# Performance work log

Hardware: AMD Instinct MI355X
Metric: run time of the kernel (lower is better)

Reference implementation:

```python
import jax, jax.numpy as jnp
import numpy as np

L = 8          # context_length
P = 196        # patches_per_frame
PT = 16        # patches_per_tactile_frame
N_EMBD = 768
N_HEAD = 12
BATCH = 4
T = (L + 1) + L * PT + L * P  # 1705


def build_mask(L, P, Pt):
    # image-query block rows (L*P rows)
    mi = np.zeros((L * P, L * P))
    a1 = np.zeros((L * P, L + 1))
    t1 = np.zeros((L * P, L * Pt))
    for i in range(L):
        mi[i * P:(i + 1) * P, :(i + 1) * P] = 1
        a1[i * P:(i + 2) * P, :i + 2] = 1
        t1[i * P:(i + 1) * P, :(i + 1) * Pt] = 1
    m1 = np.concatenate([a1, t1, mi], axis=1)
    # tactile-query block rows (L*Pt rows)
    a2 = np.zeros((L * Pt, L + 1))
    t2 = np.zeros((L * Pt, L * Pt))
    i2 = np.zeros((L * Pt, L * P))
    for i in range(L):
        a2[i * Pt:(i + 2) * Pt, :i + 2] = 1
        t2[i * Pt:(i + 1) * Pt, :(i + 1) * Pt] = 1
        i2[i * Pt:(i + 1) * Pt, :(i + 1) * P] = 1
    m2 = np.concatenate([a2, t2, i2], axis=1)
    # action-query rows (L+1 rows)
    a3 = np.zeros((L + 1, L + 1))
    t3 = np.zeros((L + 1, L * Pt))
    i3 = np.zeros((L + 1, L * P))
    for i in range(L + 1):
        a3[i:i + 2, :i + 2] = 1
        t3[i:i + 1, :(i + 1) * Pt] = 1
        i3[i:i + 1, :(i + 1) * P] = 1
    m3 = np.concatenate([a3, t3, i3], axis=1)
    return np.concatenate([m3, m2, m1], axis=0).astype(bool)


def setup_inputs() -> dict:
    key = jax.random.key(0)
    k1, k2, k3 = jax.random.split(key, 3)
    x = jax.random.normal(k1, (BATCH, T, N_EMBD), dtype=jnp.float32)
    W_attn = jax.random.normal(k2, (N_EMBD, 3 * N_EMBD), dtype=jnp.float32) * 0.02
    W_proj = jax.random.normal(k3, (N_EMBD, N_EMBD), dtype=jnp.float32) * 0.02
    mask = jnp.asarray(build_mask(L, P, PT))
    return {"x": x, "W_attn": W_attn, "W_proj": W_proj, "mask": mask, "n_head": N_HEAD}


def reference(x, W_attn, W_proj, mask, n_head):
    B, Tq, C = x.shape
    hd = C // n_head
    qkv = x @ W_attn                      # [B, T, 3C]
    q, k, v = jnp.split(qkv, 3, axis=-1)
    # [B, H, T, hd]
    q = q.reshape(B, Tq, n_head, hd).transpose(0, 2, 1, 3)
    k = k.reshape(B, Tq, n_head, hd).transpose(0, 2, 1, 3)
    v = v.reshape(B, Tq, n_head, hd).transpose(0, 2, 1, 3)
    scores = jnp.einsum("bhqd,bhkd->bhqk", q, k) / jnp.sqrt(jnp.float32(hd))
    scores = jnp.where(mask[None, None, :, :], scores, jnp.float32(-1e9))
    probs = jax.nn.softmax(scores, axis=-1)
    y = jnp.einsum("bhqk,bhkd->bhqd", probs, v)
    y = y.transpose(0, 2, 1, 3).reshape(B, Tq, C)
    return y @ W_proj
```

## Files before the change

### kernel.cpp

```cpp
#include <hip/hip_runtime.h>
#include <hip/hip_bf16.h>

typedef __attribute__((ext_vector_type(8))) short short8;
typedef __attribute__((ext_vector_type(4))) float f32x4;

#define MFMA16(a,b,c) __builtin_amdgcn_mfma_f32_16x16x32_bf16((a),(b),(c),0,0,0)

#define WAITVM(N) asm volatile("s_waitcnt vmcnt(" #N ")" ::: "memory")
#define BAR()     asm volatile("s_barrier" ::: "memory")

constexpr int Tt = 1705;
constexpr int Tp = 1792;
constexpr int NKT_ALL = 28;
constexpr int NH = 12, HD = 64, Bb = 4, C_ = 768;
constexpr int M_  = Bb * Tt;
constexpr int Mp  = 6912;
constexpr int NQT = 14;
constexpr int NCH = 4;
constexpr float QSCALE = 0.18033688011116016f;

static_assert(Mp % 256 == 0 && (3 * C_) % 256 == 0, "256-tile grid");

__device__ __forceinline__ void gl16(const void* g, void* l) {
  __builtin_amdgcn_global_load_lds((const __attribute__((address_space(1))) void*)g,
                                   (__attribute__((address_space(3))) void*)l, 16, 0, 0);
}

__device__ __forceinline__ float ex2(float x) {
  float r; asm("v_exp_f32 %0, %1" : "=v"(r) : "v"(x)); return r;
}

__device__ __forceinline__ int frame_of(int t) {
  return t < 9 ? t : (t < 137 ? ((t - 9) >> 4) : ((t - 137) / 196));
}

__device__ __forceinline__ int lim16(int a) {
  if (a >= Tt) return 0;
  int bnd = min(a + 15, Tt - 1);
  int fmax = (a == 0) ? 8 : frame_of(min(bnd, a < 137 ? 136 : bnd));
  return (fmax >= 8) ? Tt : 137 + (fmax + 1) * 196;
}

constexpr int PREP_CONV = Mp * C_ / 4 / 256;
constexpr int PREP_TA   = (C_ / 32) * (3 * C_ / 32);
constexpr int PREP_TB   = (C_ / 32) * (C_ / 32);

__global__ __launch_bounds__(256) void k_prep(const float* __restrict__ x,
                                              __hip_bfloat16* __restrict__ xb,
                                              const float* __restrict__ Wa,
                                              __hip_bfloat16* __restrict__ wat,
                                              const float* __restrict__ Wp,
                                              __hip_bfloat16* __restrict__ wpt) {
  __shared__ float tile[32][33];
  const int bid = blockIdx.x, tid = threadIdx.x;
  if (bid < PREP_CONV) {
    int i = bid * 256 + tid;
    float4 v = make_float4(0.f, 0.f, 0.f, 0.f);
    if (i * 4 < M_ * C_) v = ((const float4*)x)[i];
    __hip_bfloat16 o0 = __float2bfloat16(v.x), o1 = __float2bfloat16(v.y),
                   o2 = __float2bfloat16(v.z), o3 = __float2bfloat16(v.w);
    ushort4 u = make_ushort4(*(unsigned short*)&o0, *(unsigned short*)&o1,
                             *(unsigned short*)&o2, *(unsigned short*)&o3);
    ((ushort4*)xb)[i] = u;
    return;
  }
  const float* src; __hip_bfloat16* dst; int N, bid2;
  if (bid < PREP_CONV + PREP_TA) { bid2 = bid - PREP_CONV; src = Wa; dst = wat; N = 3 * C_; }
  else                           { bid2 = bid - PREP_CONV - PREP_TA; src = Wp; dst = wpt; N = C_; }
  const int K = C_;
  int kb = (bid2 % (C_ / 32)) * 32, nb = (bid2 / (C_ / 32)) * 32;
  int tx = tid & 31, ty = tid >> 5;
  for (int i = 0; i < 4; i++)
    tile[ty + i * 8][tx] = src[(size_t)(kb + ty + i * 8) * N + nb + tx];
  __syncthreads();
  for (int i = 0; i < 4; i++)
    dst[(size_t)(nb + ty + i * 8) * K + kb + tx] = __float2bfloat16(tile[tx][ty + i * 8]);
}

__global__ __launch_bounds__(512) void k_gemm_qkv(const __hip_bfloat16* __restrict__ xb,
                                                  const __hip_bfloat16* __restrict__ wat,
                                                  __hip_bfloat16* __restrict__ q,
                                                  __hip_bfloat16* __restrict__ kpk,
                                                  __hip_bfloat16* __restrict__ vpk) {
  __shared__ __hip_bfloat16 smem[65536];
  const int tid = threadIdx.x;
  const int lane = tid & 63, w = tid >> 6;
  const int wr = w >> 2, wc = w & 3;
  const int l16 = lane & 15, grp = lane >> 4;
  const int m0 = blockIdx.x * 256, n0 = blockIdx.y * 256;
  constexpr int NT = C_ / 32;
  constexpr int ES = 132;

  auto stage = [&](int t, int bb) {
    int k0 = t * 32;
    __hip_bfloat16* As = smem + bb * 8192;
    __hip_bfloat16* Bs = smem + 32768 + bb * 8192;
    for (int p = 0; p < 2; p++) {
      int idx = p * 512 + tid;
      int row = idx >> 2;
      int c8 = (idx & 3) ^ ((row >> 1) & 3);
      gl16(xb  + (size_t)(m0 + row) * C_ + k0 + c8 * 8, As + idx * 8);
      gl16(wat + (size_t)(n0 + row) * C_ + k0 + c8 * 8, Bs + idx * 8);
    }
  };

  f32x4 acc[8][4];
  for (int i = 0; i < 8; i++)
    for (int j = 0; j < 4; j++) { f32x4 z = {0.f,0.f,0.f,0.f}; acc[i][j] = z; }

  stage(0, 0); stage(1, 1); stage(2, 2);

  for (int t = 0; t < NT; t++) {
    if (t + 3 < NT) stage(t + 3, (t + 3) & 3);
    int rem = NT - 1 - t;
    if (rem >= 3)      WAITVM(12);
    else if (rem == 2) WAITVM(8);
    else if (rem == 1) WAITVM(4);
    else               WAITVM(0);
    BAR();
    const __hip_bfloat16* Ac = smem + (t & 3) * 8192;
    const __hip_bfloat16* Bc = smem + 32768 + (t & 3) * 8192;
    short8 bfr[4], afr[4];
    for (int nj = 0; nj < 4; nj++) {
      int row = wc * 64 + nj * 16 + l16;
      bfr[nj] = *(const short8*)(Bc + row * 32 + ((grp ^ ((row >> 1) & 3)) * 8));
    }
    for (int mi = 0; mi < 4; mi++) {
      int row = wr * 128 + mi * 16 + l16;
      afr[mi] = *(const short8*)(Ac + row * 32 + ((grp ^ ((row >> 1) & 3)) * 8));
    }
    __builtin_amdgcn_s_setprio(1);
    for (int mi = 0; mi < 4; mi++)
      for (int nj = 0; nj < 4; nj++)
        acc[mi][nj] = MFMA16(afr[mi], bfr[nj], acc[mi][nj]);
    __builtin_amdgcn_s_setprio(0);
    for (int mi = 0; mi < 4; mi++) {
      int row = wr * 128 + 64 + mi * 16 + l16;
      afr[mi] = *(const short8*)(Ac + row * 32 + ((grp ^ ((row >> 1) & 3)) * 8));
    }
    __builtin_amdgcn_s_setprio(1);
    for (int mi = 0; mi < 4; mi++)
      for (int nj = 0; nj < 4; nj++)
        acc[4 + mi][nj] = MFMA16(afr[mi], bfr[nj], acc[4 + mi][nj]);
    __builtin_amdgcn_s_setprio(0);
    BAR();
  }

  const int which = n0 / C_;
  const int cbase = n0 - which * C_;
  const int h0 = cbase >> 6;
  const float scale = (which == 0) ? QSCALE : 1.0f;
  const int b0 = m0 / Tt;
  const int b1 = min((m0 + 255) / Tt, Bb - 1);
  __hip_bfloat16* epi = smem;

  const int mmD = tid & 15, ggD = (tid >> 4) & 3;
  const int loD = (tid >> 6) & 1, hiD = tid >> 7;
  const int tinK = hiD * 16 + mmD, dK = loD * 32 + ggD * 8;
  const int dV = hiD * 16 + mmD;

  for (int pc = 0; pc < 2; pc++) {
    if ((wc >> 1) == pc) {
      int colw = (wc & 1) * 64;
      for (int mi = 0; mi < 8; mi++)
        for (int nj = 0; nj < 4; nj++) {
          int row = wr * 128 + mi * 16 + grp * 4;
          int col = colw + nj * 16 + l16;
          #pragma unroll
          for (int r = 0; r < 4; r++)
            epi[(row + r) * ES + col] = __float2bfloat16(acc[mi][nj][r] * scale);
        }
    }
    __syncthreads();
    for (int b = b0; b <= b1; b++) {
      int ts = max(0, m0 - b * Tt), te = min(Tt, m0 + 256 - b * Tt);
      if (ts >= te) continue;
      const int rb = b * Tt - m0;
      if (which == 0) {
        for (int hh = 0; hh < 2; hh++) {
          int bh = b * NH + h0 + pc * 2 + hh;
          __hip_bfloat16* qd = q + (size_t)bh * Tp * HD;
          for (int tc = ts & ~63; tc < te; tc += 64) {
            int t = tc + (tid >> 3);
            int d0 = (tid & 7) * 8;
            if (t >= ts && t < te) {
              int ad = (rb + t) * ES + hh * 64 + d0;
              union { short8 v; ushort4 h[2]; } u;
              u.h[0] = *(const ushort4*)(epi + ad);
              u.h[1] = *(const ushort4*)(epi + ad + 4);
              *(short8*)(qd + (size_t)t * HD + d0) = u.v;
            }
          }
        }
      } else if (which == 1) {
        for (int kt = ts >> 6; kt <= (te - 1) >> 6; kt++)
          for (int hh = 0; hh < 2; hh++) {
            int bh = b * NH + h0 + pc * 2 + hh;
            int t = kt * 64 + tinK;
            if (t >= ts && t < te) {
              int ad = (rb + t) * ES + hh * 64 + dK;
              union { short8 v; ushort4 h[2]; } u;
              u.h[0] = *(const ushort4*)(epi + ad);
              u.h[1] = *(const ushort4*)(epi + ad + 4);
              ((short8*)(kpk + ((size_t)bh * NKT_ALL + kt) * 4096))[tid] = u.v;
            }
          }
      } else {
        for (int kt = ts >> 6; kt <= (te - 1) >> 6; kt++)
          for (int hh = 0; hh < 2; hh++) {
            int bh = b * NH + h0 + pc * 2 + hh;
            __hip_bfloat16* vd = vpk + ((size_t)bh * NKT_ALL + kt) * 4096;
            bool full = (kt * 64 >= ts) && (kt * 64 + 64 <= te);
            if (full) {
              short8 v;
              #pragma unroll
              for (int s = 0; s < 8; s++) {
                int tin = loD * 32 + ggD * 4 + (s & 3) + ((s >> 2) << 4);
                v[s] = *(const short*)(epi + (rb + kt * 64 + tin) * ES + hh * 64 + dV);
              }
              ((short8*)vd)[tid] = v;
            } else {
              #pragma unroll
              for (int s = 0; s < 8; s++) {
                int tin = loD * 32 + ggD * 4 + (s & 3) + ((s >> 2) << 4);
                int t = kt * 64 + tin;
                if (t >= ts && t < te)
                  vd[tid * 8 + s] = epi[(rb + t) * ES + hh * 64 + dV];
              }
            }
          }
      }
    }
    __syncthreads();
  }
}

__global__ __launch_bounds__(256) void k_gemm_proj128(const __hip_bfloat16* __restrict__ A,
                                                      const __hip_bfloat16* __restrict__ Bt,
                                                      float* __restrict__ out) {
  __shared__ __hip_bfloat16 As[4][128 * 32], Bs[4][128 * 32];
  const int tid = threadIdx.x;
  const int lane = tid & 63, w = tid >> 6;
  const int wr = w >> 1, wc = w & 1;
  const int l16 = lane & 15, grp = lane >> 4;
  const int m0 = blockIdx.x * 128, n0 = blockIdx.y * 128;
  constexpr int NT = C_ / 32;

  auto stage = [&](int t, int bb) {
    int k0 = t * 32;
    for (int p = 0; p < 2; p++) {
      int idx = p * 256 + tid;
      int row = idx >> 2;
      int c8 = (idx & 3) ^ ((row >> 1) & 3);
      gl16(A  + (size_t)(m0 + row) * C_ + k0 + c8 * 8, &As[bb][idx * 8]);
      gl16(Bt + (size_t)(n0 + row) * C_ + k0 + c8 * 8, &Bs[bb][idx * 8]);
    }
  };

  f32x4 acc[4][4];
  for (int i = 0; i < 4; i++)
    for (int j = 0; j < 4; j++) { f32x4 z = {0.f,0.f,0.f,0.f}; acc[i][j] = z; }

  stage(0, 0); stage(1, 1); stage(2, 2);

  for (int t = 0; t < NT; t++) {
    if (t + 3 < NT) stage(t + 3, (t + 3) & 3);
    int rem = NT - 1 - t;
    if (rem >= 3)      WAITVM(12);
    else if (rem == 2) WAITVM(8);
    else if (rem == 1) WAITVM(4);
    else               WAITVM(0);
    BAR();
    const __hip_bfloat16* Ac = As[t & 3];
    const __hip_bfloat16* Bc = Bs[t & 3];
    short8 afr[4], bfr[4];
    for (int nj = 0; nj < 4; nj++) {
      int row = wc * 64 + nj * 16 + l16;
      bfr[nj] = *(const short8*)(Bc + row * 32 + ((grp ^ ((row >> 1) & 3)) * 8));
    }
    for (int mi = 0; mi < 4; mi++) {
      int row = wr * 64 + mi * 16 + l16;
      afr[mi] = *(const short8*)(Ac + row * 32 + ((grp ^ ((row >> 1) & 3)) * 8));
    }
    __builtin_amdgcn_s_setprio(1);
    for (int mi = 0; mi < 4; mi++)
      for (int nj = 0; nj < 4; nj++)
        acc[mi][nj] = MFMA16(afr[mi], bfr[nj], acc[mi][nj]);
    __builtin_amdgcn_s_setprio(0);
    BAR();
  }

  for (int mi = 0; mi < 4; mi++)
    for (int r = 0; r < 4; r++) {
      int m = m0 + wr * 64 + mi * 16 + grp * 4 + r;
      if (m >= M_) continue;
      for (int nj = 0; nj < 4; nj++)
        out[(size_t)m * C_ + n0 + wc * 64 + nj * 16 + l16] = acc[mi][nj][r];
    }
}

union S8u { short8 v; struct { unsigned long long lo, hi; } q; unsigned u[4]; };

__device__ __forceinline__ unsigned pack2bf(float a, float b) {
  union { __hip_bfloat162 h; unsigned u; } cv;
  cv.h = __float22bfloat162_rn(make_float2(a, b));
  return cv.u;
}

__constant__ int QLUT[NQT] = {0, 1, 11, 12, 13, 10, 8, 9, 7, 5, 6, 4, 2, 3};

__global__ __launch_bounds__(256, 2) void k_attn(const __hip_bfloat16* __restrict__ q,
                                                 const __hip_bfloat16* __restrict__ kpk,
                                                 const __hip_bfloat16* __restrict__ vpk,
                                                 __hip_bfloat16* __restrict__ Opart,
                                                 float* __restrict__ lpart) {
  const int tid = threadIdx.x, lane = tid & 63, w = tid >> 6;
  const int l16 = lane & 15, grp = lane >> 4;
  const int id = blockIdx.x;
  const int xslot = id & 7, rr_ = id >> 3;
  const int bh = xslot + 8 * (rr_ / 56);
  const int cqs = rr_ % 56;
  const int qt = QLUT[cqs >> 2], ch = cqs & (NCH - 1);
  const int cq = qt * NCH + ch;
  const int t0q = qt * 128;
  const __hip_bfloat16* qb = q + (size_t)bh * Tp * HD;

  int lim[2], Cmn[2], Ath[2], Bth[2], Cth[2];
  for (int g = 0; g < 2; g++) {
    int a = t0q + w * 32 + g * 16;
    lim[g] = lim16(a);
    int fqmn, fql;
    if (a >= Tt) { fqmn = 8; fql = 8; }
    else {
      int bnd = min(a + 15, Tt - 1);
      fqmn = min(frame_of(a), frame_of(bnd));
      int t = a + l16;
      fql = (t >= Tt) ? 8 : frame_of(t);
    }
    Cmn[g] = min(137 + 196 * (fqmn + 1), Tt);
    Ath[g] = fql + 2;
    Bth[g] = 9 + 16 * (fql + 1);
    Cth[g] = min(137 + 196 * (fql + 1), Tt);
  }
  int limw = max(lim[0], lim[1]);
  int nktw = (limw + 63) >> 6;
  int k0t = (ch * nktw) >> 2;
  int k1t = ((ch + 1) * nktw) >> 2;

  short8 qa[2][2];
  for (int g = 0; g < 2; g++) {
    const __hip_bfloat16* qr = qb + (size_t)(t0q + w * 32 + g * 16 + l16) * HD + grp * 8;
    qa[g][0] = *(const short8*)(qr);
    qa[g][1] = *(const short8*)(qr + 32);
  }
  f32x4 o[2][4];
  for (int g = 0; g < 2; g++)
    for (int jt = 0; jt < 4; jt++) { f32x4 z = {0.f,0.f,0.f,0.f}; o[g][jt] = z; }
  f32x4 ps[2];
  { f32x4 z = {0.f,0.f,0.f,0.f}; ps[0] = z; ps[1] = z; }

  const short8* kbase = (const short8*)(kpk + (size_t)bh * NKT_ALL * 4096);
  const short8* vbase = (const short8*)(vpk + (size_t)bh * NKT_ALL * 4096);

  for (int kt = k0t; kt < k1t; kt++) {
    const int t0k = kt * 64;
    const short8* kp = kbase + (size_t)kt * 512;
    const short8* vp = vbase + (size_t)kt * 512;
    short8 kf[4][2], vf[4][2];
    for (int j = 0; j < 4; j++)
      for (int hh = 0; hh < 2; hh++) kf[j][hh] = kp[(j * 2 + hh) * 64 + lane];
    for (int jt = 0; jt < 4; jt++)
      for (int kb2 = 0; kb2 < 2; kb2++) vf[jt][kb2] = vp[(jt * 2 + kb2) * 64 + lane];

    f32x4 s[2][4];
    for (int j = 0; j < 4; j++) {
      f32x4 z = {0.f,0.f,0.f,0.f};
      s[0][j] = MFMA16(kf[j][0], qa[0][0], z);
      s[0][j] = MFMA16(kf[j][1], qa[0][1], s[0][j]);
      s[1][j] = MFMA16(kf[j][0], qa[1][0], z);
      s[1][j] = MFMA16(kf[j][1], qa[1][1], s[1][j]);
    }

    bool act0 = t0k < lim[0], act1 = t0k < lim[1];
    bool fullk = (t0k + 64 <= Tt);
    S8u pf[2][2];
    for (int g = 0; g < 2; g++) {
      bool act = g == 0 ? act0 : act1;
      if (!act) continue;
      bool needm = !(fullk && (t0k >= 192 ? (t0k + 64) <= Cmn[g] : Cmn[g] >= Tt));
      if (needm) {
        for (int j = 0; j < 4; j++)
          for (int r = 0; r < 4; r++) {
            int key = t0k + j * 16 + grp * 4 + r;
            int thr = key < 9 ? Ath[g] : (key < 137 ? Bth[g] : Cth[g]);
            if (key >= thr) s[g][j][r] = -1e30f;
          }
      }
      f32x4 p[4];
      for (int j = 0; j < 4; j++)
        for (int r = 0; r < 4; r++) p[j][r] = ex2(s[g][j][r]);
      ps[g] += (p[0] + p[1]) + (p[2] + p[3]);
      pf[g][0].u[0] = pack2bf(p[0][0], p[0][1]);
      pf[g][0].u[1] = pack2bf(p[0][2], p[0][3]);
      pf[g][0].u[2] = pack2bf(p[1][0], p[1][1]);
      pf[g][0].u[3] = pack2bf(p[1][2], p[1][3]);
      pf[g][1].u[0] = pack2bf(p[2][0], p[2][1]);
      pf[g][1].u[1] = pack2bf(p[2][2], p[2][3]);
      pf[g][1].u[2] = pack2bf(p[3][0], p[3][1]);
      pf[g][1].u[3] = pack2bf(p[3][2], p[3][3]);
    }

    for (int jt = 0; jt < 4; jt++)
      for (int kb2 = 0; kb2 < 2; kb2++) {
        if (act0) o[0][jt] = MFMA16(vf[jt][kb2], pf[0][kb2].v, o[0][jt]);
        if (act1) o[1][jt] = MFMA16(vf[jt][kb2], pf[1][kb2].v, o[1][jt]);
      }
  }

  float lr[2];
  for (int g = 0; g < 2; g++) {
    float sum = (ps[g][0] + ps[g][1]) + (ps[g][2] + ps[g][3]);
    sum += __shfl_xor(sum, 16);
    sum += __shfl_xor(sum, 32);
    lr[g] = sum;
  }

  const int blk = bh * (NQT * NCH) + cq;
  __hip_bfloat16* op = Opart + (size_t)blk * (128 * 64);
  for (int g = 0; g < 2; g++) {
    int row = w * 32 + g * 16 + l16;
    for (int jt = 0; jt < 4; jt++) {
      unsigned p01 = pack2bf(o[g][jt][0], o[g][jt][1]);
      unsigned p23 = pack2bf(o[g][jt][2], o[g][jt][3]);
      ushort4 u;
      u.x = p01 & 0xffff; u.y = p01 >> 16; u.z = p23 & 0xffff; u.w = p23 >> 16;
      *(ushort4*)(op + row * 64 + jt * 16 + grp * 4) = u;
    }
    if (grp == 0) lpart[(size_t)blk * 128 + w * 32 + g * 16 + l16] = lr[g];
  }
}

__global__ __launch_bounds__(256) void k_combine(const __hip_bfloat16* __restrict__ Opart,
                                                 const float* __restrict__ lpart,
                                                 __hip_bfloat16* __restrict__ y) {
  const int tid = threadIdx.x;
  const int qt = blockIdx.x, bh = blockIdx.y;
  const int b = bh / NH, h = bh - b * NH;
  const int t0q = qt * 128;
  const int blk0 = bh * (NQT * NCH) + qt * NCH;
  __shared__ float ls[128];
  if (tid < 128) {
    float s = 0.f;
    for (int c = 0; c < NCH; c++) s += lpart[(size_t)(blk0 + c) * 128 + tid];
    ls[tid] = (s > 0.f) ? 1.0f / s : 0.f;
  }
  __syncthreads();
  for (int it = 0; it < 4; it++) {
    int e8 = it * 256 + tid;
    int e = e8 * 8;
    int row = e >> 6, d = e & 63;
    int t = t0q + row;
    if (t >= Tt) continue;
    float acc[8] = {0,0,0,0,0,0,0,0};
    for (int c = 0; c < NCH; c++) {
      short8 vv = *(const short8*)(Opart + (size_t)(blk0 + c) * (128 * 64) + e);
      for (int i = 0; i < 8; i++) {
        union { unsigned u; float f; } cv;
        cv.u = ((unsigned)(unsigned short)vv[i]) << 16;
        acc[i] += cv.f;
      }
    }
    float rinv = ls[row];
    short8 outv;
    for (int i = 0; i < 8; i += 2) {
      unsigned p = pack2bf(acc[i] * rinv, acc[i + 1] * rinv);
      outv[i] = (short)(p & 0xffff);
      outv[i + 1] = (short)(p >> 16);
    }
    *(short8*)(y + (size_t)(b * Tt + t) * C_ + h * 64 + d) = outv;
  }
}

extern "C" void kernel_launch(void* const* d_in, const int* in_sizes, int n_in,
                              void* d_out, int out_size, void* d_ws, size_t ws_size,
                              hipStream_t stream) {
  const float* x  = (const float*)d_in[0];
  const float* Wa = (const float*)d_in[1];
  const float* Wp = (const float*)d_in[2];
  float* out = (float*)d_out;

  char* ws = (char*)d_ws;
  size_t off = 0;
  auto alloc = [&](size_t bytes) { size_t r = off; off += (bytes + 255) & ~(size_t)255; return r; };
  __hip_bfloat16* xb  = (__hip_bfloat16*)(ws + alloc((size_t)Mp * C_ * 2));
  __hip_bfloat16* wat = (__hip_bfloat16*)(ws + alloc((size_t)3 * C_ * C_ * 2));
  __hip_bfloat16* wpt = (__hip_bfloat16*)(ws + alloc((size_t)C_ * C_ * 2));
  __hip_bfloat16* qb  = (__hip_bfloat16*)(ws + alloc((size_t)Bb * NH * Tp * HD * 2));
  __hip_bfloat16* kpk = (__hip_bfloat16*)(ws + alloc((size_t)Bb * NH * NKT_ALL * 4096 * 2));
  __hip_bfloat16* vpk = (__hip_bfloat16*)(ws + alloc((size_t)Bb * NH * NKT_ALL * 4096 * 2));
  __hip_bfloat16* yb  = (__hip_bfloat16*)(ws + alloc((size_t)Mp * C_ * 2));
  __hip_bfloat16* Opart = (__hip_bfloat16*)(ws + alloc((size_t)Bb * NH * NQT * NCH * 128 * 64 * 2));
  float*          lpart = (float*)(ws + alloc((size_t)Bb * NH * NQT * NCH * 128 * 4));

  k_prep<<<PREP_CONV + PREP_TA + PREP_TB, 256, 0, stream>>>(x, xb, Wa, wat, Wp, wpt);
  k_gemm_qkv<<<dim3(Mp / 256, 3 * C_ / 256), 512, 0, stream>>>(xb, wat, qb, kpk, vpk);
  k_attn<<<dim3(Bb * NH * NQT * NCH), 256, 0, stream>>>(qb, kpk, vpk, Opart, lpart);
  k_combine<<<dim3(NQT, Bb * NH), 256, 0, stream>>>(Opart, lpart, yb);
  k_gemm_proj128<<<dim3(Mp / 128, C_ / 128), 256, 0, stream>>>(yb, wpt, out);
}
```

Before: 203.8 us.

## Interleave next-tile global-to-LDS loads with MFMA phases in QKV GEMM

Splits each K-step of the QKV projection GEMM into four phases. Each phase reads two A fragments, issues one slice of the prefetch loads for tile t+3, and runs a block of MFMAs, instead of issuing the whole prefetch up front. The aim is to spread global-load issue across compute so it overlaps better with MFMA work. In exchange it adds more barriers per K-step (two per phase) and explicit lgkmcnt waits. The vmcnt thresholds are lowered to match the changed issue order.

```diff
diff --git a/kernel.cpp b/kernel.cpp
--- a/kernel.cpp
+++ b/kernel.cpp
@@ -8,6 +8,7 @@
 
 #define WAITVM(N) asm volatile("s_waitcnt vmcnt(" #N ")" ::: "memory")
 #define BAR()     asm volatile("s_barrier" ::: "memory")
+#define LGKM0()   asm volatile("s_waitcnt lgkmcnt(0)" ::: "memory")
 
 constexpr int Tt = 1705;
 constexpr int Tp = 1792;
@@ -111,39 +112,49 @@
   stage(0, 0); stage(1, 1); stage(2, 2);
 
   for (int t = 0; t < NT; t++) {
-    if (t + 3 < NT) stage(t + 3, (t + 3) & 3);
     int rem = NT - 1 - t;
-    if (rem >= 3)      WAITVM(12);
-    else if (rem == 2) WAITVM(8);
+    if (rem >= 2)      WAITVM(8);
     else if (rem == 1) WAITVM(4);
     else               WAITVM(0);
     BAR();
     const __hip_bfloat16* Ac = smem + (t & 3) * 8192;
     const __hip_bfloat16* Bc = smem + 32768 + (t & 3) * 8192;
-    short8 bfr[4], afr[4];
-    for (int nj = 0; nj < 4; nj++) {
-      int row = wc * 64 + nj * 16 + l16;
-      bfr[nj] = *(const short8*)(Bc + row * 32 + ((grp ^ ((row >> 1) & 3)) * 8));
-    }
-    for (int mi = 0; mi < 4; mi++) {
-      int row = wr * 128 + mi * 16 + l16;
-      afr[mi] = *(const short8*)(Ac + row * 32 + ((grp ^ ((row >> 1) & 3)) * 8));
-    }
-    __builtin_amdgcn_s_setprio(1);
-    for (int mi = 0; mi < 4; mi++)
+    const bool pre = (t + 3 < NT);
+    const int k3 = (t + 3) * 32;
+    __hip_bfloat16* As3 = smem + ((t + 3) & 3) * 8192;
+    __hip_bfloat16* Bs3 = smem + 32768 + ((t + 3) & 3) * 8192;
+    short8 bfr[4];
+    #pragma unroll
+    for (int p = 0; p < 4; p++) {
+      if (p == 0) {
+        for (int nj = 0; nj < 4; nj++) {
+          int row = wc * 64 + nj * 16 + l16;
+          bfr[nj] = *(const short8*)(Bc + row * 32 + ((grp ^ ((row >> 1) & 3)) * 8));
+        }
+      }
+      int row0 = wr * 128 + p * 32 + l16;
+      short8 a0 = *(const short8*)(Ac + row0 * 32 + ((grp ^ ((row0 >> 1) & 3)) * 8));
+      int row1 = row0 + 16;
+      short8 a1 = *(const short8*)(Ac + row1 * 32 + ((grp ^ ((row1 >> 1) & 3)) * 8));
+      if (pre) {
+        int idx = (p >> 1) * 512 + tid;
+        int row = idx >> 2;
+        int c8 = (idx & 3) ^ ((row >> 1) & 3);
+        if ((p & 1) == 0)
+          gl16(xb  + (size_t)(m0 + row) * C_ + k3 + c8 * 8, As3 + idx * 8);
+        else
+          gl16(wat + (size_t)(n0 + row) * C_ + k3 + c8 * 8, Bs3 + idx * 8);
+      }
+      BAR();
+      LGKM0();
+      __builtin_amdgcn_s_setprio(1);
       for (int nj = 0; nj < 4; nj++)
-        acc[mi][nj] = MFMA16(afr[mi], bfr[nj], acc[mi][nj]);
-    __builtin_amdgcn_s_setprio(0);
-    for (int mi = 0; mi < 4; mi++) {
-      int row = wr * 128 + 64 + mi * 16 + l16;
-      afr[mi] = *(const short8*)(Ac + row * 32 + ((grp ^ ((row >> 1) & 3)) * 8));
-    }
-    __builtin_amdgcn_s_setprio(1);
-    for (int mi = 0; mi < 4; mi++)
+        acc[2 * p][nj] = MFMA16(a0, bfr[nj], acc[2 * p][nj]);
       for (int nj = 0; nj < 4; nj++)
-        acc[4 + mi][nj] = MFMA16(afr[mi], bfr[nj], acc[4 + mi][nj]);
-    __builtin_amdgcn_s_setprio(0);
-    BAR();
+        acc[2 * p + 1][nj] = MFMA16(a1, bfr[nj], acc[2 * p + 1][nj]);
+      __builtin_amdgcn_s_setprio(0);
+      BAR();
+    }
   }
 
   const int which = n0 / C_;
```

Result: no change. 204.3 us (+0.2%).
